# Kernel optimization log

Hardware: AMD Instinct MI355X
Metric: run time of the kernel (lower is better)

Reference implementation:

```python
import jax, jax.numpy as jnp
import numpy as np

KERNEL_SIZE = 13
SIGMA_MIN, SIGMA_MAX = 0.4, 10.0
BETA, THRESHOLD = 0.95, 1.0


@jax.custom_vjp
def spike(x):
    # Heaviside forward, snntorch ATan surrogate backward (alpha=2)
    return (x > 0).astype(x.dtype)

def _spike_fwd(x):
    return spike(x), x

def _spike_bwd(x, g):
    return (g / (1.0 + (jnp.pi * x) ** 2),)

spike.defvjp(_spike_fwd, _spike_bwd)


def setup_inputs() -> dict:
    key = jax.random.key(0)
    k1, k2 = jax.random.split(key)
    B, C, T = 32, 224, 2048
    inp = jax.random.normal(k1, (B, 1, C, T), dtype=jnp.float32)
    linear_w = jax.random.normal(k2, (1, C), dtype=jnp.float32) * (1.0 / np.sqrt(C))
    return {"inp": inp, "linear_w": linear_w}


def _forward(inp, linear_w):
    x = inp[:, 0]  # [B, C, T]
    B, C, T = x.shape
    sigma_mean = 0.5 * (SIGMA_MIN + SIGMA_MAX)
    # adaptive sigma per (batch, time): Linear over channel axis, no bias
    w = sigma_mean + jnp.einsum('bct,c->bt', x, linear_w[0]) * (SIGMA_MAX - SIGMA_MIN)
    w = jnp.clip(w, SIGMA_MIN, SIGMA_MAX)  # [B, T]

    half = KERNEL_SIZE // 2
    r = jnp.linspace(-half, half, KERNEL_SIZE)
    r_all = jnp.linspace(-half * 10, half * 10, KERNEL_SIZE * 10)
    sig = w[..., None]  # [B, T, 1]
    kern = jnp.exp(-0.5 * (r / sig) ** 2)                       # [B, T, K]
    norm = jnp.exp(-0.5 * (r_all / sig) ** 2).sum(-1, keepdims=True)
    kern = kern / norm                                          # normalized over fine grid

    # adaptive gaussian smoothing along the CHANNEL axis (per timestep kernel)
    xt = jnp.transpose(x, (0, 2, 1))                            # [B, T, C]
    padded = jnp.pad(xt, ((0, 0), (0, 0), (half, half)))        # zero pad channels
    x_mean = sum(padded[:, :, k:k + C] * kern[:, :, k:k + 1]
                 for k in range(KERNEL_SIZE))                   # [B, T, C]
    x_mean = jnp.transpose(x_mean, (0, 2, 1))                   # [B, C, T]

    I = x - jax.nn.relu(x - x_mean)                             # soft min(x, x_mean)

    # Leaky-integrate-and-fire over time (snntorch Leaky, reset-by-subtract)
    def step(mem, I_t):
        reset = jax.lax.stop_gradient((mem > THRESHOLD).astype(I_t.dtype))
        mem = BETA * mem + I_t - reset * THRESHOLD
        spk = spike(mem - THRESHOLD)
        return mem, spk

    I_seq = jnp.transpose(I, (2, 0, 1))                         # [T, B, C]
    _, spk = jax.lax.scan(step, jnp.zeros((B, C), I.dtype), I_seq)
    spk = jnp.transpose(spk, (1, 2, 0))                         # [B, C, T]
    return spk[:, None]                                         # [B, 1, C, T]


def reference(inp, linear_w):
    return _forward(inp, linear_w)
```

## Files before the change

### kernel.cpp

```cpp
#include <hip/hip_runtime.h>
#include <math.h>

#define BB 32
#define CCH 224
#define TTT 2048
#define TPB 64
#define NT  (TTT/TPB)
#define CG  28
#define NCG (CCH/CG)
#define ROWS 40
#define XROW 68
#define IROW 29
#define CPW 4
#define CTH 448

__device__ __forceinline__ void bar_lds() {
    asm volatile("s_waitcnt lgkmcnt(0)" ::: "memory");
    __builtin_amdgcn_s_barrier();
    asm volatile("" ::: "memory");
}

__global__ __launch_bounds__(256) void kw(
    const float* __restrict__ x, const float* __restrict__ lw,
    double* __restrict__ kernG)
{
    __shared__ double sp[4][64];
    const int b  = blockIdx.y;
    const int tl = threadIdx.x & 63;
    const int q  = threadIdx.x >> 6;
    const int t  = blockIdx.x * 64 + tl;

    const float* xb  = x + (((size_t)(b * CCH + 56 * q)) << 11) + t;
    const float* lwq = lw + 56 * q;

    double p = 0.0;
    #pragma unroll 8
    for (int i = 0; i < 56; ++i)
        p += (double)xb[(size_t)i << 11] * (double)lwq[i];
    sp[q][tl] = p;
    __syncthreads();

    if (threadIdx.x < 64) {
        double acc = (sp[0][tl] + sp[1][tl]) + (sp[2][tl] + sp[3][tl]);

        double w = 5.2 + acc * 9.6;
        w = fmin(fmax(w, 0.4), 10.0);
        double iw2 = 1.0 / (w * w);

        const double s = 120.0 / 129.0;
        double G  = exp(-0.125 * s * s * iw2);
        double G2 = G * G, G4 = G2 * G2, G8 = G4 * G4;
        double term = G, cmul = G8, norm = G;
        for (int u = 1; u <= 64; ++u) { term *= cmul; cmul *= G8; norm += term; }
        norm *= 2.0;

        double P = exp(-0.5 * iw2), P2 = P * P;
        double a = 1.0, bm = P, inv = 1.0 / norm;
        double* kr = kernG + (size_t)(b * TTT + t) * 7;
        kr[0] = inv;
        #pragma unroll
        for (int d = 1; d <= 6; ++d) {
            a *= bm; bm *= P2;
            kr[d] = a * inv;
        }
    }
}

__global__ __launch_bounds__(512) void kf(
    const float* __restrict__ x, const double* __restrict__ kernG,
    float* __restrict__ out)
{
    __shared__ __align__(16) float xs[2][ROWS][XROW];
    __shared__ double kd[2][TPB][7];
    __shared__ double Is[2][TPB][IROW];
    __shared__ unsigned long long bitsb[2][CG];

    const int b   = blockIdx.y;
    const int cgi = blockIdx.x;
    const int c0  = cgi * CG;
    const int tid = threadIdx.x;
    const int ctid = tid - 64;

    const float*  xbase = x + (((size_t)(b * CCH)) << 11);
    const double* kbase = kernG + (size_t)(b * TTT) * 7;
    float* obase = out + (((size_t)(b * CCH + c0)) << 11);

    double mem = 0.0;
    bool   r   = false;

    float4 rv[2]; double kv[7];

    if (tid >= 64) {
        #pragma unroll
        for (int i2 = 0; i2 < 2; ++i2) {
            int e = ctid + i2 * CTH;
            if (e < ROWS * 16) {
                int rr = e >> 4, q = e & 15;
                int cr = c0 - 6 + rr;
                float4 v = make_float4(0.f, 0.f, 0.f, 0.f);
                if (cr >= 0 && cr < CCH)
                    v = *(const float4*)(xbase + ((size_t)cr << 11) + 4 * q);
                *(float4*)&xs[0][rr][4 * q] = v;
            }
        }
        if (ctid < TPB) {
            const double* kp = kbase + (size_t)ctid * 7;
            #pragma unroll
            for (int i2 = 0; i2 < 7; ++i2) kd[0][ctid][i2] = kp[i2];
        }
        {
            const int gt0 = TPB;
            #pragma unroll
            for (int i2 = 0; i2 < 2; ++i2) {
                int e = ctid + i2 * CTH;
                if (e < ROWS * 16) {
                    int rr = e >> 4, q = e & 15;
                    int cr = c0 - 6 + rr;
                    rv[i2] = make_float4(0.f, 0.f, 0.f, 0.f);
                    if (cr >= 0 && cr < CCH)
                        rv[i2] = *(const float4*)(xbase + ((size_t)cr << 11) + gt0 + 4 * q);
                }
            }
            if (ctid < TPB) {
                const double* kp = kbase + (size_t)(gt0 + ctid) * 7;
                #pragma unroll
                for (int i2 = 0; i2 < 7; ++i2) kv[i2] = kp[i2];
            }
        }
    }
    bar_lds();

    for (int k = 0; k <= NT + 1; ++k) {
        if (tid >= 64) {
            const int buf = k & 1, nbuf = (k + 1) & 1;
            if (k + 1 <= NT - 1) {
                #pragma unroll
                for (int i2 = 0; i2 < 2; ++i2) {
                    int e = ctid + i2 * CTH;
                    if (e < ROWS * 16) {
                        int rr = e >> 4, q = e & 15;
                        *(float4*)&xs[nbuf][rr][4 * q] = rv[i2];
                    }
                }
                if (ctid < TPB) {
                    #pragma unroll
                    for (int i2 = 0; i2 < 7; ++i2) kd[nbuf][ctid][i2] = kv[i2];
                }
            }
            if (k + 2 <= NT - 1) {
                const int gt0 = (k + 2) * TPB;
                #pragma unroll
                for (int i2 = 0; i2 < 2; ++i2) {
                    int e = ctid + i2 * CTH;
                    if (e < ROWS * 16) {
                        int rr = e >> 4, q = e & 15;
                        int cr = c0 - 6 + rr;
                        rv[i2] = make_float4(0.f, 0.f, 0.f, 0.f);
                        if (cr >= 0 && cr < CCH)
                            rv[i2] = *(const float4*)(xbase + ((size_t)cr << 11) + gt0 + 4 * q);
                    }
                }
                if (ctid < TPB) {
                    const double* kp = kbase + (size_t)(gt0 + ctid) * 7;
                    #pragma unroll
                    for (int i2 = 0; i2 < 7; ++i2) kv[i2] = kp[i2];
                }
            }
            if (k >= 2) {
                const int j = k - 2, jb = j & 1;
                const int t0o = j * TPB;
                int c = ctid >> 4, q = ctid & 15;
                unsigned long long bits = bitsb[jb][c] >> (4 * q);
                float4 v;
                v.x = (bits & 1ull) ? 1.0f : 0.0f;
                v.y = (bits & 2ull) ? 1.0f : 0.0f;
                v.z = (bits & 4ull) ? 1.0f : 0.0f;
                v.w = (bits & 8ull) ? 1.0f : 0.0f;
                *(float4*)(obase + ((size_t)c << 11) + t0o + 4 * q) = v;
            }
            if (k <= NT - 1) {
                const int t  = ctid & 63;
                const int g  = ctid >> 6;
                const int cb = CPW * g;
                double kk7[7];
                #pragma unroll
                for (int i2 = 0; i2 < 7; ++i2) kk7[i2] = kd[buf][t][i2];
                double xv[13];
                #pragma unroll
                for (int i2 = 0; i2 < 13; ++i2) xv[i2] = (double)xs[buf][cb + i2][t];
                #pragma unroll
                for (int c = 0; c < CPW; ++c) {
                    double acc = 0.0;
                    #pragma unroll
                    for (int kk2 = 0; kk2 < 13; ++kk2) {
                        int d = kk2 < 6 ? 6 - kk2 : kk2 - 6;
                        acc = fma(xv[(c + kk2) % 13], kk7[d], acc);
                    }
                    double xvv = xv[(c + 6) % 13];
                    double dd  = xvv - acc;
                    Is[buf][t][cb + c] = xvv - (dd > 0.0 ? dd : 0.0);
                    if (c < CPW - 1) xv[c % 13] = (double)xs[buf][cb + c + 13][t];
                }
            }
        } else {
            if (k >= 1 && k <= NT) {
                const int p = (k - 1) & 1;
                const int c = tid;
                __builtin_amdgcn_s_setprio(1);
                if (c < CG) {
                    unsigned long long bits = 0ull;
                    double va[8], vb[8], ca[8], cb2[8];
                    #pragma unroll
                    for (int j2 = 0; j2 < 8; ++j2) va[j2] = Is[p][j2][c];
                    #pragma unroll
                    for (int j2 = 0; j2 < 8; ++j2) ca[j2] = va[j2] - 1.0;
                    #pragma unroll
                    for (int g = 0; g < 64; g += 16) {
                        #pragma unroll
                        for (int j2 = 0; j2 < 8; ++j2) vb[j2] = Is[p][g + 8 + j2][c];
                        #pragma unroll
                        for (int j2 = 0; j2 < 8; ++j2) cb2[j2] = vb[j2] - 1.0;
                        #pragma unroll
                        for (int j2 = 0; j2 < 8; ++j2) {
                            double ax = r ? ca[j2] : va[j2];
                            mem = fma(0.95, mem, ax);
                            r = mem > 1.0;
                            bits |= (unsigned long long)(r ? 1 : 0) << (g + j2);
                        }
                        if (g + 16 < 64) {
                            #pragma unroll
                            for (int j2 = 0; j2 < 8; ++j2) va[j2] = Is[p][g + 16 + j2][c];
                            #pragma unroll
                            for (int j2 = 0; j2 < 8; ++j2) ca[j2] = va[j2] - 1.0;
                        }
                        #pragma unroll
                        for (int j2 = 0; j2 < 8; ++j2) {
                            double ax = r ? cb2[j2] : vb[j2];
                            mem = fma(0.95, mem, ax);
                            r = mem > 1.0;
                            bits |= (unsigned long long)(r ? 1 : 0) << (g + 8 + j2);
                        }
                    }
                    bitsb[p][c] = bits;
                }
                __builtin_amdgcn_s_setprio(0);
            }
        }
        bar_lds();
    }
}

extern "C" void kernel_launch(void* const* d_in, const int* in_sizes, int n_in,
                              void* d_out, int out_size, void* d_ws, size_t ws_size,
                              hipStream_t stream)
{
    const float* x  = (const float*)d_in[0];
    const float* lw = (const float*)d_in[1];
    float* out = (float*)d_out;

    double* kernG = (double*)d_ws;

    kw<<<dim3(TTT / 64, BB), 256, 0, stream>>>(x, lw, kernG);
    kf<<<dim3(NCG, BB), 512, 0, stream>>>(x, kernG, out);
}
```

Before: 146.0 us.

## Load smoothing inputs directly into registers, double time tile, speculate LIF fma

Removes the LDS staging of x and kernel weights in the fused kernel. Each compute thread now loads its own 16-channel halo column and 7 weights straight from global memory into two alternating register sets, with a two-deep prefetch. The time tile grows to 128, so there are half as many barrier phases, and each channel emits two 64-bit spike masks per tile. The serial LIF recurrence now computes both reset and no-reset fma candidates and selects one, which shortens the dependency chain. In exchange, overlapping halo rows are loaded redundantly per thread group, the loads are scalar and strided, and register pressure rises.

```diff
diff --git a/kernel.cpp b/kernel.cpp
--- a/kernel.cpp
+++ b/kernel.cpp
@@ -4,15 +4,12 @@
 #define BB 32
 #define CCH 224
 #define TTT 2048
-#define TPB 64
+#define TPB 128
 #define NT  (TTT/TPB)
 #define CG  28
 #define NCG (CCH/CG)
-#define ROWS 40
-#define XROW 68
 #define IROW 29
 #define CPW 4
-#define CTH 448
 
 __device__ __forceinline__ void bar_lds() {
     asm volatile("s_waitcnt lgkmcnt(0)" ::: "memory");
@@ -70,10 +67,8 @@
     const float* __restrict__ x, const double* __restrict__ kernG,
     float* __restrict__ out)
 {
-    __shared__ __align__(16) float xs[2][ROWS][XROW];
-    __shared__ double kd[2][TPB][7];
     __shared__ double Is[2][TPB][IROW];
-    __shared__ unsigned long long bitsb[2][CG];
+    __shared__ unsigned long long bitsb[2][CG][2];
 
     const int b   = blockIdx.y;
     const int cgi = blockIdx.x;
@@ -88,165 +83,134 @@
     double mem = 0.0;
     bool   r   = false;
 
-    float4 rv[2]; double kv[7];
-
-    if (tid >= 64) {
+    const int tl = ctid & 63;
+    const int g  = ctid >> 6;
+    const int cb = CPW * g;
+
+    auto issue = [&](int tile, float (&rv)[2][16], double (&kv)[2][7]) {
+        const int gt0 = tile * TPB;
         #pragma unroll
-        for (int i2 = 0; i2 < 2; ++i2) {
-            int e = ctid + i2 * CTH;
-            if (e < ROWS * 16) {
-                int rr = e >> 4, q = e & 15;
-                int cr = c0 - 6 + rr;
-                float4 v = make_float4(0.f, 0.f, 0.f, 0.f);
-                if (cr >= 0 && cr < CCH)
-                    v = *(const float4*)(xbase + ((size_t)cr << 11) + 4 * q);
-                *(float4*)&xs[0][rr][4 * q] = v;
-            }
+        for (int h = 0; h < 2; ++h) {
+            const int tt = gt0 + tl + 64 * h;
+            #pragma unroll
+            for (int i = 0; i < 16; ++i) {
+                int cr = c0 + cb - 6 + i;
+                rv[h][i] = (cr >= 0 && cr < CCH)
+                         ? xbase[((size_t)cr << 11) + tt] : 0.f;
+            }
+            const double* kp = kbase + (size_t)tt * 7;
+            #pragma unroll
+            for (int i = 0; i < 7; ++i) kv[h][i] = kp[i];
         }
-        if (ctid < TPB) {
-            const double* kp = kbase + (size_t)ctid * 7;
-            #pragma unroll
-            for (int i2 = 0; i2 < 7; ++i2) kd[0][ctid][i2] = kp[i2];
-        }
-        {
-            const int gt0 = TPB;
-            #pragma unroll
-            for (int i2 = 0; i2 < 2; ++i2) {
-                int e = ctid + i2 * CTH;
-                if (e < ROWS * 16) {
-                    int rr = e >> 4, q = e & 15;
-                    int cr = c0 - 6 + rr;
-                    rv[i2] = make_float4(0.f, 0.f, 0.f, 0.f);
-                    if (cr >= 0 && cr < CCH)
-                        rv[i2] = *(const float4*)(xbase + ((size_t)cr << 11) + gt0 + 4 * q);
-                }
-            }
-            if (ctid < TPB) {
-                const double* kp = kbase + (size_t)(gt0 + ctid) * 7;
-                #pragma unroll
-                for (int i2 = 0; i2 < 7; ++i2) kv[i2] = kp[i2];
-            }
-        }
-    }
-    bar_lds();
-
-    for (int k = 0; k <= NT + 1; ++k) {
+    };
+
+    auto phase = [&](int k, float (&rv)[2][16], double (&kv)[2][7]) {
         if (tid >= 64) {
-            const int buf = k & 1, nbuf = (k + 1) & 1;
-            if (k + 1 <= NT - 1) {
-                #pragma unroll
-                for (int i2 = 0; i2 < 2; ++i2) {
-                    int e = ctid + i2 * CTH;
-                    if (e < ROWS * 16) {
-                        int rr = e >> 4, q = e & 15;
-                        *(float4*)&xs[nbuf][rr][4 * q] = rv[i2];
-                    }
-                }
-                if (ctid < TPB) {
-                    #pragma unroll
-                    for (int i2 = 0; i2 < 7; ++i2) kd[nbuf][ctid][i2] = kv[i2];
-                }
-            }
-            if (k + 2 <= NT - 1) {
-                const int gt0 = (k + 2) * TPB;
-                #pragma unroll
-                for (int i2 = 0; i2 < 2; ++i2) {
-                    int e = ctid + i2 * CTH;
-                    if (e < ROWS * 16) {
-                        int rr = e >> 4, q = e & 15;
-                        int cr = c0 - 6 + rr;
-                        rv[i2] = make_float4(0.f, 0.f, 0.f, 0.f);
-                        if (cr >= 0 && cr < CCH)
-                            rv[i2] = *(const float4*)(xbase + ((size_t)cr << 11) + gt0 + 4 * q);
-                    }
-                }
-                if (ctid < TPB) {
-                    const double* kp = kbase + (size_t)(gt0 + ctid) * 7;
-                    #pragma unroll
-                    for (int i2 = 0; i2 < 7; ++i2) kv[i2] = kp[i2];
-                }
-            }
+            const int buf = k & 1;
             if (k >= 2) {
                 const int j = k - 2, jb = j & 1;
                 const int t0o = j * TPB;
-                int c = ctid >> 4, q = ctid & 15;
-                unsigned long long bits = bitsb[jb][c] >> (4 * q);
-                float4 v;
-                v.x = (bits & 1ull) ? 1.0f : 0.0f;
-                v.y = (bits & 2ull) ? 1.0f : 0.0f;
-                v.z = (bits & 4ull) ? 1.0f : 0.0f;
-                v.w = (bits & 8ull) ? 1.0f : 0.0f;
-                *(float4*)(obase + ((size_t)c << 11) + t0o + 4 * q) = v;
+                const int c = ctid >> 4, q = ctid & 15;
+                #pragma unroll
+                for (int h = 0; h < 2; ++h) {
+                    unsigned long long bits = bitsb[jb][c][h] >> (4 * q);
+                    float4 v;
+                    v.x = (bits & 1ull) ? 1.0f : 0.0f;
+                    v.y = (bits & 2ull) ? 1.0f : 0.0f;
+                    v.z = (bits & 4ull) ? 1.0f : 0.0f;
+                    v.w = (bits & 8ull) ? 1.0f : 0.0f;
+                    *(float4*)(obase + ((size_t)c << 11) + t0o + 64 * h + 4 * q) = v;
+                }
             }
             if (k <= NT - 1) {
-                const int t  = ctid & 63;
-                const int g  = ctid >> 6;
-                const int cb = CPW * g;
-                double kk7[7];
                 #pragma unroll
-                for (int i2 = 0; i2 < 7; ++i2) kk7[i2] = kd[buf][t][i2];
-                double xv[13];
-                #pragma unroll
-                for (int i2 = 0; i2 < 13; ++i2) xv[i2] = (double)xs[buf][cb + i2][t];
-                #pragma unroll
-                for (int c = 0; c < CPW; ++c) {
-                    double acc = 0.0;
-                    #pragma unroll
-                    for (int kk2 = 0; kk2 < 13; ++kk2) {
-                        int d = kk2 < 6 ? 6 - kk2 : kk2 - 6;
-                        acc = fma(xv[(c + kk2) % 13], kk7[d], acc);
+                for (int h = 0; h < 2; ++h) {
+                    double kk7[7];
+                    #pragma unroll
+                    for (int i = 0; i < 7; ++i) kk7[i] = kv[h][i];
+                    double xv[16];
+                    #pragma unroll
+                    for (int i = 0; i < 16; ++i) xv[i] = (double)rv[h][i];
+                    #pragma unroll
+                    for (int c = 0; c < CPW; ++c) {
+                        double acc = 0.0;
+                        #pragma unroll
+                        for (int kk = 0; kk < 13; ++kk) {
+                            int d = kk < 6 ? 6 - kk : kk - 6;
+                            acc = fma(xv[c + kk], kk7[d], acc);
+                        }
+                        double xvv = xv[c + 6];
+                        double dd  = xvv - acc;
+                        Is[buf][tl + 64 * h][cb + c] = xvv - (dd > 0.0 ? dd : 0.0);
                     }
-                    double xvv = xv[(c + 6) % 13];
-                    double dd  = xvv - acc;
-                    Is[buf][t][cb + c] = xvv - (dd > 0.0 ? dd : 0.0);
-                    if (c < CPW - 1) xv[c % 13] = (double)xs[buf][cb + c + 13][t];
                 }
             }
+            if (k + 2 <= NT - 1) issue(k + 2, rv, kv);
         } else {
             if (k >= 1 && k <= NT) {
                 const int p = (k - 1) & 1;
                 const int c = tid;
                 __builtin_amdgcn_s_setprio(1);
                 if (c < CG) {
-                    unsigned long long bits = 0ull;
-                    double va[8], vb[8], ca[8], cb2[8];
+                    unsigned long long bits0 = 0ull, bits1 = 0ull;
+                    double va[8], vb8[8], ca[8], cb2[8];
                     #pragma unroll
                     for (int j2 = 0; j2 < 8; ++j2) va[j2] = Is[p][j2][c];
                     #pragma unroll
                     for (int j2 = 0; j2 < 8; ++j2) ca[j2] = va[j2] - 1.0;
                     #pragma unroll
-                    for (int g = 0; g < 64; g += 16) {
-                        #pragma unroll
-                        for (int j2 = 0; j2 < 8; ++j2) vb[j2] = Is[p][g + 8 + j2][c];
-                        #pragma unroll
-                        for (int j2 = 0; j2 < 8; ++j2) cb2[j2] = vb[j2] - 1.0;
+                    for (int g2 = 0; g2 < TPB; g2 += 16) {
+                        #pragma unroll
+                        for (int j2 = 0; j2 < 8; ++j2) vb8[j2] = Is[p][g2 + 8 + j2][c];
+                        #pragma unroll
+                        for (int j2 = 0; j2 < 8; ++j2) cb2[j2] = vb8[j2] - 1.0;
                         #pragma unroll
                         for (int j2 = 0; j2 < 8; ++j2) {
-                            double ax = r ? ca[j2] : va[j2];
-                            mem = fma(0.95, mem, ax);
+                            double m1 = fma(0.95, mem, va[j2]);
+                            double m2 = fma(0.95, mem, ca[j2]);
+                            mem = r ? m2 : m1;
                             r = mem > 1.0;
-                            bits |= (unsigned long long)(r ? 1 : 0) << (g + j2);
-                        }
-                        if (g + 16 < 64) {
+                            const int s = g2 + j2;
+                            if (s < 64) bits0 |= (unsigned long long)(r ? 1 : 0) << s;
+                            else        bits1 |= (unsigned long long)(r ? 1 : 0) << (s - 64);
+                        }
+                        if (g2 + 16 < TPB) {
                             #pragma unroll
-                            for (int j2 = 0; j2 < 8; ++j2) va[j2] = Is[p][g + 16 + j2][c];
+                            for (int j2 = 0; j2 < 8; ++j2) va[j2] = Is[p][g2 + 16 + j2][c];
                             #pragma unroll
                             for (int j2 = 0; j2 < 8; ++j2) ca[j2] = va[j2] - 1.0;
                         }
                         #pragma unroll
                         for (int j2 = 0; j2 < 8; ++j2) {
-                            double ax = r ? cb2[j2] : vb[j2];
-                            mem = fma(0.95, mem, ax);
+                            double m1 = fma(0.95, mem, vb8[j2]);
+                            double m2 = fma(0.95, mem, cb2[j2]);
+                            mem = r ? m2 : m1;
                             r = mem > 1.0;
-                            bits |= (unsigned long long)(r ? 1 : 0) << (g + 8 + j2);
+                            const int s = g2 + 8 + j2;
+                            if (s < 64) bits0 |= (unsigned long long)(r ? 1 : 0) << s;
+                            else        bits1 |= (unsigned long long)(r ? 1 : 0) << (s - 64);
                         }
                     }
-                    bitsb[p][c] = bits;
+                    bitsb[p][c][0] = bits0;
+                    bitsb[p][c][1] = bits1;
                 }
                 __builtin_amdgcn_s_setprio(0);
             }
         }
         bar_lds();
+    };
+
+    float  rA[2][16], rB[2][16];
+    double kA[2][7],  kB[2][7];
+
+    if (tid >= 64) {
+        issue(0, rA, kA);
+        issue(1, rB, kB);
+    }
+
+    for (int kk = 0; kk < NT + 2; kk += 2) {
+        phase(kk,     rA, kA);
+        phase(kk + 1, rB, kB);
     }
 }
 
```

Result: no change. 145.4 us (-0.4%).
